# Optimization experiments

Hardware: AMD Instinct MI355X
Metric: run time of the kernel (lower is better)

The kernel has to match this reference:

```python
import jax, jax.numpy as jnp
import numpy as np

D = 512; N = 4096; NH = 16; DEPTH = 3; MLP = 4; GENES = 250; GH = 64; GW = 64


def setup_inputs() -> dict:
    key = jax.random.key(0)
    ks = jax.random.split(key, 10)
    gf = jax.random.normal(ks[0], (N, D), jnp.float32)
    # unique spot positions: permutation of the 64x64 grid cells
    perm = jax.random.permutation(ks[1], GH * GW)[:N]
    coords = jnp.stack([perm // GW, perm % GW], axis=1).astype(jnp.int32)
    s = 0.02
    rn = lambda k, sh: jax.random.normal(k, sh, jnp.float32) * s
    return dict(
        global_feats=gf, coords=coords, grid_h=GH, grid_w=GW,
        ln1_g=jnp.ones((DEPTH, D)), ln1_b=jnp.zeros((DEPTH, D)),
        wqkv=rn(ks[2], (DEPTH, 3 * D, D)), bqkv=jnp.zeros((DEPTH, 3 * D)),
        wo=rn(ks[3], (DEPTH, D, D)), bo=jnp.zeros((DEPTH, D)),
        ln2_g=jnp.ones((DEPTH, D)), ln2_b=jnp.zeros((DEPTH, D)),
        w1=rn(ks[4], (DEPTH, MLP * D, D)), b1=jnp.zeros((DEPTH, MLP * D)),
        w2=rn(ks[5], (DEPTH, D, MLP * D)), b2=jnp.zeros((DEPTH, D)),
        ck=rn(ks[6], (DEPTH, D, 1, 3, 3)), cb=jnp.zeros((DEPTH, D)),
        lnf_g=jnp.ones((D,)), lnf_b=jnp.zeros((D,)),
        wp=rn(ks[7], (GENES, D)), bp=jnp.zeros((GENES,)),
    )


def _ln(x, g, b, eps=1e-5):
    m = jnp.mean(x, axis=-1, keepdims=True)
    v = jnp.var(x, axis=-1, keepdims=True)
    return (x - m) * jax.lax.rsqrt(v + eps) * g + b


def reference(global_feats, coords, grid_h, grid_w, ln1_g, ln1_b, wqkv, bqkv,
              wo, bo, ln2_g, ln2_b, w1, b1, w2, b2, ck, cb, lnf_g, lnf_b, wp, bp):
    x = global_feats  # [N, D]
    n, d = x.shape
    nh = NH; dh = d // nh
    rows = coords[:, 0]; cols = coords[:, 1]
    for i in range(ln1_g.shape[0]):
        # --- self-attention (eval mode, dropout off) ---
        xn = _ln(x, ln1_g[i], ln1_b[i])
        qkv = xn @ wqkv[i].T + bqkv[i]                      # [N, 3D]
        q, k, v = jnp.split(qkv, 3, axis=-1)
        q = q.reshape(n, nh, dh).transpose(1, 0, 2)        # [H, N, dh]
        k = k.reshape(n, nh, dh).transpose(1, 0, 2)
        v = v.reshape(n, nh, dh).transpose(1, 0, 2)
        att = jax.nn.softmax(jnp.einsum('hqd,hkd->hqk', q, k) * (dh ** -0.5), axis=-1)
        ao = jnp.einsum('hqk,hkd->hqd', att, v).transpose(1, 0, 2).reshape(n, d)
        x = x + (ao @ wo[i].T + bo[i])
        # --- MLP ---
        h = jax.nn.gelu(_ln(x, ln2_g[i], ln2_b[i]) @ w1[i].T + b1[i], approximate=False)
        x = x + (h @ w2[i].T + b2[i])
        # --- APEG: scatter -> depthwise conv -> gather ---
        grid = jnp.zeros((d, grid_h, grid_w), x.dtype).at[:, rows, cols].set(x.T)
        co = jax.lax.conv_general_dilated(
            grid[None], ck[i], window_strides=(1, 1), padding=((1, 1), (1, 1)),
            dimension_numbers=('NCHW', 'OIHW', 'NCHW'), feature_group_count=d)[0]
        co = co + cb[i][:, None, None]
        x = x + co[:, rows, cols].T
    x = _ln(x, lnf_g, lnf_b)
    pred = x @ wp.T + bp
    return (x, pred)
```

## Files before the change

### kernel.cpp

```cpp
#include <hip/hip_runtime.h>
#include <math.h>

#define D 512
#define N_TOK 4096
#define NHEAD 16
#define DH 32
#define DEPTH 3
#define MLPD 2048
#define GENES 250
#define GH 64
#define GW 64

typedef __attribute__((ext_vector_type(8))) short short8;
typedef __attribute__((ext_vector_type(4))) float f32x4;
typedef unsigned short ushort_t;

#define AS1 __attribute__((address_space(1)))
#define AS3 __attribute__((address_space(3)))

#if defined(__has_builtin)
#if __has_builtin(__builtin_amdgcn_exp2f)
#define EXP2F(x) __builtin_amdgcn_exp2f(x)
#endif
#endif
#ifndef EXP2F
#define EXP2F(x) __expf(0.69314718056f * (x))
#endif

__device__ __forceinline__ unsigned short f2bf(float f) {
  unsigned int u = __float_as_uint(f);
  u += 0x7fffu + ((u >> 16) & 1u);
  return (unsigned short)(u >> 16);
}
__device__ __forceinline__ unsigned int bfpack(float a, float b) {
  return __builtin_amdgcn_perm(__float_as_uint(b), __float_as_uint(a), 0x07060302u);
}
__device__ __forceinline__ void gload_lds16(const ushort_t* g, ushort_t* l) {
  __builtin_amdgcn_global_load_lds(
      (const AS1 unsigned int*)g,
      (AS3 unsigned int*)(unsigned int)(unsigned long long)l, 16, 0, 0);
}
__device__ __forceinline__ int perm64(int m) {
  int mi = m >> 4, g = (m >> 2) & 3, r = m & 3;
  return ((mi & 1) << 5) | (g << 3) | ((mi >> 1) << 2) | r;
}

__global__ __launch_bounds__(256) void ln_kernel(const float* __restrict__ x,
    const float* __restrict__ g, const float* __restrict__ b,
    float* __restrict__ yf, ushort_t* __restrict__ ybf) {
  int row = blockIdx.x;
  int t = threadIdx.x;
  const float* xr = x + (size_t)row * D;
  float v0 = xr[t], v1 = xr[t + 256];
  float s = v0 + v1;
  float sq = v0 * v0 + v1 * v1;
#pragma unroll
  for (int off = 32; off > 0; off >>= 1) {
    s += __shfl_down(s, off, 64);
    sq += __shfl_down(sq, off, 64);
  }
  __shared__ float s1[4], s2[4];
  int wid = t >> 6, lane = t & 63;
  if (lane == 0) { s1[wid] = s; s2[wid] = sq; }
  __syncthreads();
  float tot = s1[0] + s1[1] + s1[2] + s1[3];
  float totq = s2[0] + s2[1] + s2[2] + s2[3];
  float mean = tot * (1.0f / D);
  float var = totq * (1.0f / D) - mean * mean;
  float rs = rsqrtf(var + 1e-5f);
  float r0 = (v0 - mean) * rs * g[t] + b[t];
  float r1 = (v1 - mean) * rs * g[t + 256] + b[t + 256];
  if (yf) { yf[(size_t)row * D + t] = r0; yf[(size_t)row * D + t + 256] = r1; }
  if (ybf) {
    ybf[(size_t)row * D + t] = f2bf(r0);
    ybf[(size_t)row * D + t + 256] = f2bf(r1);
  }
}

#define GBK 32

template <int TM, int TN>
__global__ __launch_bounds__(256) void gemm_bf(
    const ushort_t* __restrict__ A, const ushort_t* __restrict__ B,
    const float* __restrict__ bias, const float* __restrict__ res,
    float* __restrict__ C, ushort_t* __restrict__ Cbf,
    ushort_t* __restrict__ qO, ushort_t* __restrict__ kO, ushort_t* __restrict__ vO,
    int K, int ldc, int nstore, int mode) {
  constexpr int MI = TM / 32;
  constexpr int NI = TN / 32;
  __shared__ ushort_t As[TM * GBK];
  __shared__ ushort_t Bs[TN * GBK];
  int t = threadIdx.x;
  int w = t >> 6, lane = t & 63;
  int g = lane >> 4, c = lane & 15;
  int bm = blockIdx.y * TM, bn = blockIdx.x * TN;
  int wr = (w >> 1) * (TM / 2);
  int wc = (w & 1) * (TN / 2);

  const ushort_t* ga0 = A + (size_t)(bm + (t >> 2)) * K + (t & 3) * 8;
  const ushort_t* gb0 = B + (size_t)(bn + (t >> 2)) * K + (t & 3) * 8;
  const ushort_t* ga1 = A + (size_t)(bm + 64 + (t >> 2)) * K + (t & 3) * 8;
  const ushort_t* gb1 = B + (size_t)(bn + 64 + (t >> 2)) * K + (t & 3) * 8;
  ushort_t* la0 = As + t * 8;
  ushort_t* lb0 = Bs + t * 8;

  f32x4 acc[MI][NI] = {};

  for (int k0 = 0; k0 < K; k0 += GBK) {
    gload_lds16(ga0, la0);
    gload_lds16(gb0, lb0);
    if (TM == 128) gload_lds16(ga1, As + (t + 256) * 8);
    if (TN == 128) gload_lds16(gb1, Bs + (t + 256) * 8);
    ga0 += GBK; gb0 += GBK; ga1 += GBK; gb1 += GBK;
    __syncthreads();

    short8 af[MI], bfr[NI];
#pragma unroll
    for (int mi = 0; mi < MI; ++mi)
      af[mi] = *(const short8*)&As[(wr + mi * 16 + c) * GBK + g * 8];
#pragma unroll
    for (int ni = 0; ni < NI; ++ni)
      bfr[ni] = *(const short8*)&Bs[(wc + ni * 16 + c) * GBK + g * 8];
#pragma unroll
    for (int mi = 0; mi < MI; ++mi)
#pragma unroll
      for (int ni = 0; ni < NI; ++ni)
        acc[mi][ni] = __builtin_amdgcn_mfma_f32_16x16x32_bf16(
            af[mi], bfr[ni], acc[mi][ni], 0, 0, 0);
    __syncthreads();
  }

  const float qs_scale = 0.17677669529663688f * 1.4426950408889634f;
#pragma unroll
  for (int ni = 0; ni < NI; ++ni) {
    int col = bn + wc + ni * 16 + c;
    float bv = bias[col];
    bool cok = col < nstore;
#pragma unroll
    for (int mi = 0; mi < MI; ++mi) {
      int row0 = bm + wr + mi * 16 + g * 4;
#pragma unroll
      for (int reg = 0; reg < 4; ++reg) {
        int row = row0 + reg;
        float v = acc[mi][ni][reg] + bv;
        if (mode == 0) {
          size_t idx = (size_t)row * ldc + col;
          if (cok) {
            if (res) v += res[idx];
            C[idx] = v;
          }
        } else if (mode == 1) {
          v = 0.5f * v * (1.0f + erff(v * 0.70710678118654752f));
          Cbf[(size_t)row * ldc + col] = f2bf(v);
        } else {
          int which = col >> 9;
          int h = (col >> 5) & 15;
          int d = col & 31;
          size_t hb = (size_t)h * (N_TOK * DH);
          if (which == 0)
            qO[hb + (size_t)row * DH + d] = f2bf(v * qs_scale);
          else if (which == 1)
            kO[hb + (size_t)row * DH + d] = f2bf(v);
          else
            vO[hb + (size_t)d * N_TOK + ((row & ~63) | perm64(row & 63))] = f2bf(v);
        }
      }
    }
  }
}

#define KST 40
#define VTST 72

__global__ __launch_bounds__(256) void attn_mfma(
    const ushort_t* __restrict__ qb, const ushort_t* __restrict__ kb,
    const ushort_t* __restrict__ vtb, ushort_t* __restrict__ ao) {
  __shared__ ushort_t Ks[64 * KST];
  __shared__ ushort_t Vts[32 * VTST];
  int qt = blockIdx.x, head = blockIdx.y;
  int t = threadIdx.x;
  int w = t >> 6, lane = t & 63;
  int g = lane >> 4, c = lane & 15;
  const size_t hbase = (size_t)head * (N_TOK * DH);
  int q0 = qt * 128 + w * 32;

  short8 qf[2];
  qf[0] = *(const short8*)(qb + hbase + (size_t)(q0 + c) * DH + g * 8);
  qf[1] = *(const short8*)(qb + hbase + (size_t)(q0 + 16 + c) * DH + g * 8);

  short8 ones;
#pragma unroll
  for (int i = 0; i < 8; ++i) ones[i] = (short)0x3F80;

  f32x4 o[2][2] = {};
  f32x4 lf[2] = {};
  const f32x4 zf = {0.f, 0.f, 0.f, 0.f};

  const ushort_t* kg = kb + hbase + (size_t)(t >> 2) * DH + (t & 3) * 8;
  const ushort_t* vg = vtb + hbase + (size_t)(t >> 3) * N_TOK + (t & 7) * 8;
  ushort_t* kw = &Ks[(t >> 2) * KST + (t & 3) * 8];
  ushort_t* vw = &Vts[(t >> 3) * VTST + (t & 7) * 8];

  short8 kreg = *(const short8*)kg;
  short8 vreg = *(const short8*)vg;

  typedef union { short8 s8; unsigned int u32[4]; } pk_t;

  for (int tile = 0; tile < N_TOK / 64; ++tile) {
    __syncthreads();
    *(short8*)kw = kreg;
    *(short8*)vw = vreg;
    __syncthreads();
    if (tile + 1 < N_TOK / 64) {
      kreg = *(const short8*)(kg + (size_t)(tile + 1) * 64 * DH);
      vreg = *(const short8*)(vg + (tile + 1) * 64);
    }

    short8 kf[4];
#pragma unroll
    for (int mi = 0; mi < 4; ++mi)
      kf[mi] = *(const short8*)&Ks[(mi * 16 + c) * KST + g * 8];
    short8 vf[2][2];
#pragma unroll
    for (int half = 0; half < 2; ++half)
#pragma unroll
      for (int ch = 0; ch < 2; ++ch)
        vf[half][ch] = *(const short8*)&Vts[(half * 16 + c) * VTST + ch * 32 + g * 8];

    short8 pf[2][2];
#pragma unroll
    for (int qs = 0; qs < 2; ++qs) {
      f32x4 sp[4];
#pragma unroll
      for (int mi = 0; mi < 4; ++mi)
        sp[mi] = __builtin_amdgcn_mfma_f32_16x16x32_bf16(kf[mi], qf[qs], zf, 0, 0, 0);
      float pr[4][4];
#pragma unroll
      for (int mi = 0; mi < 4; ++mi)
#pragma unroll
        for (int r = 0; r < 4; ++r) pr[mi][r] = EXP2F(sp[mi][r]);
      pk_t p0, p1;
      p0.u32[0] = bfpack(pr[0][0], pr[0][1]);
      p0.u32[1] = bfpack(pr[0][2], pr[0][3]);
      p0.u32[2] = bfpack(pr[2][0], pr[2][1]);
      p0.u32[3] = bfpack(pr[2][2], pr[2][3]);
      p1.u32[0] = bfpack(pr[1][0], pr[1][1]);
      p1.u32[1] = bfpack(pr[1][2], pr[1][3]);
      p1.u32[2] = bfpack(pr[3][0], pr[3][1]);
      p1.u32[3] = bfpack(pr[3][2], pr[3][3]);
      pf[qs][0] = p0.s8;
      pf[qs][1] = p1.s8;
    }

#pragma unroll
    for (int qs = 0; qs < 2; ++qs) {
#pragma unroll
      for (int ch = 0; ch < 2; ++ch) {
        lf[qs] = __builtin_amdgcn_mfma_f32_16x16x32_bf16(ones, pf[qs][ch], lf[qs], 0, 0, 0);
#pragma unroll
        for (int half = 0; half < 2; ++half)
          o[qs][half] = __builtin_amdgcn_mfma_f32_16x16x32_bf16(
              vf[half][ch], pf[qs][ch], o[qs][half], 0, 0, 0);
      }
    }
  }

#pragma unroll
  for (int qs = 0; qs < 2; ++qs) {
    float inv = 1.0f / lf[qs][0];
    int q = q0 + qs * 16 + c;
    ushort_t* op = ao + (size_t)q * D + head * DH;
#pragma unroll
    for (int half = 0; half < 2; ++half)
#pragma unroll
      for (int reg = 0; reg < 4; ++reg)
        op[half * 16 + g * 4 + reg] = f2bf(o[qs][half][reg] * inv);
  }
}

__global__ void scatter_kernel(const int* __restrict__ coords,
                               int* __restrict__ pos2tok) {
  int n = blockIdx.x * 256 + threadIdx.x;
  if (n < N_TOK) pos2tok[coords[2 * n] * GW + coords[2 * n + 1]] = n;
}

__global__ __launch_bounds__(256) void conv_ln_kernel(
    const float* __restrict__ xin, float* __restrict__ xout,
    const float* __restrict__ ck, const float* __restrict__ cb,
    const int* __restrict__ pos2tok, const int* __restrict__ coords,
    const float* __restrict__ g, const float* __restrict__ b,
    float* __restrict__ yf, ushort_t* __restrict__ ybf) {
  int n = blockIdx.x, t = threadIdx.x;
  __shared__ int nb[9];
  if (t < 9) {
    int r = coords[2 * n], c = coords[2 * n + 1];
    int dy = t / 3 - 1, dx = t % 3 - 1;
    int rr = r + dy, cc = c + dx;
    nb[t] = (rr >= 0 && rr < GH && cc >= 0 && cc < GW) ? pos2tok[rr * GW + cc] : -1;
  }
  __syncthreads();
  float v[2];
#pragma unroll
  for (int j = 0; j < 2; ++j) {
    int ch = t + j * 256;
    float s = cb[ch];
#pragma unroll
    for (int tap = 0; tap < 9; ++tap) {
      int tok = nb[tap];
      if (tok >= 0) s = fmaf(ck[ch * 9 + tap], xin[(size_t)tok * D + ch], s);
    }
    v[j] = xin[(size_t)n * D + ch] + s;
    xout[(size_t)n * D + ch] = v[j];
  }
  float s = v[0] + v[1];
  float sq = v[0] * v[0] + v[1] * v[1];
#pragma unroll
  for (int off = 32; off > 0; off >>= 1) {
    s += __shfl_down(s, off, 64);
    sq += __shfl_down(sq, off, 64);
  }
  __shared__ float s1[4], s2[4];
  int wid = t >> 6, lane = t & 63;
  if (lane == 0) { s1[wid] = s; s2[wid] = sq; }
  __syncthreads();
  float tot = s1[0] + s1[1] + s1[2] + s1[3];
  float totq = s2[0] + s2[1] + s2[2] + s2[3];
  float mean = tot * (1.0f / D);
  float var = totq * (1.0f / D) - mean * mean;
  float rs = rsqrtf(var + 1e-5f);
  float r0 = (v[0] - mean) * rs * g[t] + b[t];
  float r1 = (v[1] - mean) * rs * g[t + 256] + b[t + 256];
  if (yf) { yf[(size_t)n * D + t] = r0; yf[(size_t)n * D + t + 256] = r1; }
  ybf[(size_t)n * D + t] = f2bf(r0);
  ybf[(size_t)n * D + t + 256] = f2bf(r1);
}

__global__ __launch_bounds__(256) void castw(const float* __restrict__ src,
    ushort_t* __restrict__ dst, int n_src, int n_dst) {
  int i = (blockIdx.x * 256 + threadIdx.x) * 4;
  if (i >= n_dst) return;
  unsigned long long pk = 0;
#pragma unroll
  for (int j = 0; j < 4; ++j) {
    float v = (i + j < n_src) ? src[i + j] : 0.f;
    pk |= ((unsigned long long)f2bf(v)) << (16 * j);
  }
  *(unsigned long long*)(dst + i) = pk;
}

__global__ void pad_bias(const float* __restrict__ src, float* __restrict__ dst) {
  int i = threadIdx.x;
  dst[i] = (i < GENES) ? src[i] : 0.f;
}

extern "C" void kernel_launch(void* const* d_in, const int* in_sizes, int n_in,
                              void* d_out, int out_size, void* d_ws, size_t ws_size,
                              hipStream_t stream) {
  const float* gf     = (const float*)d_in[0];
  const int*   coords = (const int*)d_in[1];
  const float* ln1_g  = (const float*)d_in[4];
  const float* ln1_b  = (const float*)d_in[5];
  const float* wqkv   = (const float*)d_in[6];
  const float* bqkv   = (const float*)d_in[7];
  const float* wo     = (const float*)d_in[8];
  const float* bo     = (const float*)d_in[9];
  const float* ln2_g  = (const float*)d_in[10];
  const float* ln2_b  = (const float*)d_in[11];
  const float* w1     = (const float*)d_in[12];
  const float* b1     = (const float*)d_in[13];
  const float* w2     = (const float*)d_in[14];
  const float* b2     = (const float*)d_in[15];
  const float* ck     = (const float*)d_in[16];
  const float* cb     = (const float*)d_in[17];
  const float* lnf_g  = (const float*)d_in[18];
  const float* lnf_b  = (const float*)d_in[19];
  const float* wp     = (const float*)d_in[20];
  const float* bp     = (const float*)d_in[21];
  float* out = (float*)d_out;

  const size_t ND = (size_t)N_TOK * D;
  float* xb0 = (float*)d_ws;
  float* xb1 = xb0 + ND;
  ushort_t* xn_bf  = (ushort_t*)(xb1 + ND);
  ushort_t* ao_bf  = xn_bf + ND;
  ushort_t* out_bf = ao_bf + ND;
  ushort_t* shared = out_bf + ND;
  ushort_t* qb   = shared;
  ushort_t* kbuf = qb + ND;
  ushort_t* vtb  = kbuf + ND;
  ushort_t* h_bf = shared;
  ushort_t* wqkv_bf = shared + (size_t)N_TOK * MLPD;
  ushort_t* wo_bf = wqkv_bf + DEPTH * 3 * D * D;
  ushort_t* w1_bf = wo_bf + DEPTH * D * D;
  ushort_t* w2_bf = w1_bf + DEPTH * MLPD * D;
  ushort_t* wp_bf = w2_bf + DEPTH * D * MLPD;
  float* bp_pad = (float*)(wp_bf + 256 * D);
  int* pos2tok = (int*)(bp_pad + 256);

  hipMemcpyAsync(xb0, gf, ND * sizeof(float), hipMemcpyDeviceToDevice, stream);
  hipMemsetAsync(pos2tok, 0xFF, GH * GW * sizeof(int), stream);
  scatter_kernel<<<(N_TOK + 255) / 256, 256, 0, stream>>>(coords, pos2tok);

  int nw;
  nw = DEPTH * 3 * D * D;  castw<<<(nw / 4 + 255) / 256, 256, 0, stream>>>(wqkv, wqkv_bf, nw, nw);
  nw = DEPTH * D * D;      castw<<<(nw / 4 + 255) / 256, 256, 0, stream>>>(wo, wo_bf, nw, nw);
  nw = DEPTH * MLPD * D;   castw<<<(nw / 4 + 255) / 256, 256, 0, stream>>>(w1, w1_bf, nw, nw);
  nw = DEPTH * D * MLPD;   castw<<<(nw / 4 + 255) / 256, 256, 0, stream>>>(w2, w2_bf, nw, nw);
  castw<<<(256 * D / 4 + 255) / 256, 256, 0, stream>>>(wp, wp_bf, GENES * D, 256 * D);
  pad_bias<<<1, 256, 0, stream>>>(bp, bp_pad);

  ln_kernel<<<N_TOK, 256, 0, stream>>>(xb0, ln1_g, ln1_b, nullptr, xn_bf);

  float* x  = xb0;
  float* xo = xb1;
  for (int i = 0; i < DEPTH; ++i) {
    gemm_bf<128, 128><<<dim3(12, 32), 256, 0, stream>>>(
        xn_bf, wqkv_bf + (size_t)i * 3 * D * D, bqkv + (size_t)i * 3 * D,
        nullptr, nullptr, nullptr, qb, kbuf, vtb, D, 0, 3 * D, 2);
    attn_mfma<<<dim3(N_TOK / 128, NHEAD), 256, 0, stream>>>(qb, kbuf, vtb, ao_bf);
    gemm_bf<64, 64><<<dim3(8, 64), 256, 0, stream>>>(
        ao_bf, wo_bf + (size_t)i * D * D, bo + (size_t)i * D,
        x, x, nullptr, nullptr, nullptr, nullptr, D, D, D, 0);
    ln_kernel<<<N_TOK, 256, 0, stream>>>(x, ln2_g + i * D, ln2_b + i * D, nullptr, xn_bf);
    gemm_bf<128, 128><<<dim3(16, 32), 256, 0, stream>>>(
        xn_bf, w1_bf + (size_t)i * MLPD * D, b1 + (size_t)i * MLPD,
        nullptr, nullptr, h_bf, nullptr, nullptr, nullptr, D, MLPD, MLPD, 1);
    gemm_bf<64, 64><<<dim3(8, 64), 256, 0, stream>>>(
        h_bf, w2_bf + (size_t)i * D * MLPD, b2 + (size_t)i * D,
        x, x, nullptr, nullptr, nullptr, nullptr, MLPD, D, D, 0);
    if (i < DEPTH - 1) {
      conv_ln_kernel<<<N_TOK, 256, 0, stream>>>(
          x, xo, ck + (size_t)i * D * 9, cb + (size_t)i * D, pos2tok, coords,
          ln1_g + (i + 1) * D, ln1_b + (i + 1) * D, nullptr, xn_bf);
    } else {
      conv_ln_kernel<<<N_TOK, 256, 0, stream>>>(
          x, xo, ck + (size_t)i * D * 9, cb + (size_t)i * D, pos2tok, coords,
          lnf_g, lnf_b, out, out_bf);
    }
    float* tmp = x; x = xo; xo = tmp;
  }
  gemm_bf<64, 64><<<dim3(4, 64), 256, 0, stream>>>(
      out_bf, wp_bf, bp_pad, nullptr, out + ND, nullptr, nullptr, nullptr, nullptr,
      D, GENES, GENES, 0);
}
```

Measured before the change: 714.4 us.

## Double-buffer GEMM LDS tiles and vectorize V-transpose stores in QKV epilogue

Turns the bf16 GEMM main loop into a double-buffered pipeline. The global-to-LDS loads for the next K tile are issued before the MFMAs on the current one, leaving one barrier per iteration instead of two. The 64x64 GEMMs stage two K halves (64 wide) per buffer to cut loop and sync overhead. The QKV epilogue is split into its own path that packs four bf16 V values into a single 8-byte store using the inlined permutation, in exchange for doubled LDS use and more code complexity.

After: 624.2 us. -12.6%, faster.

```diff
diff --git a/kernel.cpp b/kernel.cpp
--- a/kernel.cpp
+++ b/kernel.cpp
@@ -77,9 +77,7 @@
   }
 }
 
-#define GBK 32
-
-template <int TM, int TN>
+template <int TM, int TN, int NKH>
 __global__ __launch_bounds__(256) void gemm_bf(
     const ushort_t* __restrict__ A, const ushort_t* __restrict__ B,
     const float* __restrict__ bias, const float* __restrict__ res,
@@ -88,8 +86,8 @@
     int K, int ldc, int nstore, int mode) {
   constexpr int MI = TM / 32;
   constexpr int NI = TN / 32;
-  __shared__ ushort_t As[TM * GBK];
-  __shared__ ushort_t Bs[TN * GBK];
+  __shared__ ushort_t As[2][NKH][TM * 32];
+  __shared__ ushort_t Bs[2][NKH][TN * 32];
   int t = threadIdx.x;
   int w = t >> 6, lane = t & 63;
   int g = lane >> 4, c = lane & 15;
@@ -97,40 +95,88 @@
   int wr = (w >> 1) * (TM / 2);
   int wc = (w & 1) * (TN / 2);
 
-  const ushort_t* ga0 = A + (size_t)(bm + (t >> 2)) * K + (t & 3) * 8;
-  const ushort_t* gb0 = B + (size_t)(bn + (t >> 2)) * K + (t & 3) * 8;
-  const ushort_t* ga1 = A + (size_t)(bm + 64 + (t >> 2)) * K + (t & 3) * 8;
-  const ushort_t* gb1 = B + (size_t)(bn + 64 + (t >> 2)) * K + (t & 3) * 8;
-  ushort_t* la0 = As + t * 8;
-  ushort_t* lb0 = Bs + t * 8;
+  const ushort_t* gA = A + (size_t)(bm + (t >> 2)) * K + (t & 3) * 8;
+  const ushort_t* gB = B + (size_t)(bn + (t >> 2)) * K + (t & 3) * 8;
+
+  auto stage = [&](int p, int koff) {
+#pragma unroll
+    for (int h = 0; h < NKH; ++h) {
+      gload_lds16(gA + koff + h * 32, &As[p][h][t * 8]);
+      if (TM == 128)
+        gload_lds16(gA + koff + h * 32 + (size_t)64 * K, &As[p][h][(t + 256) * 8]);
+      gload_lds16(gB + koff + h * 32, &Bs[p][h][t * 8]);
+      if (TN == 128)
+        gload_lds16(gB + koff + h * 32 + (size_t)64 * K, &Bs[p][h][(t + 256) * 8]);
+    }
+  };
 
   f32x4 acc[MI][NI] = {};
 
-  for (int k0 = 0; k0 < K; k0 += GBK) {
-    gload_lds16(ga0, la0);
-    gload_lds16(gb0, lb0);
-    if (TM == 128) gload_lds16(ga1, As + (t + 256) * 8);
-    if (TN == 128) gload_lds16(gb1, Bs + (t + 256) * 8);
-    ga0 += GBK; gb0 += GBK; ga1 += GBK; gb1 += GBK;
+  const int niter = K / (32 * NKH);
+  stage(0, 0);
+  __syncthreads();
+  for (int it = 0; it < niter; ++it) {
+    int p = it & 1;
+    if (it + 1 < niter) stage(p ^ 1, (it + 1) * 32 * NKH);
+#pragma unroll
+    for (int kh = 0; kh < NKH; ++kh) {
+      short8 af[MI], bfr[NI];
+#pragma unroll
+      for (int mi = 0; mi < MI; ++mi)
+        af[mi] = *(const short8*)&As[p][kh][(wr + mi * 16 + c) * 32 + g * 8];
+#pragma unroll
+      for (int ni = 0; ni < NI; ++ni)
+        bfr[ni] = *(const short8*)&Bs[p][kh][(wc + ni * 16 + c) * 32 + g * 8];
+#pragma unroll
+      for (int mi = 0; mi < MI; ++mi)
+#pragma unroll
+        for (int ni = 0; ni < NI; ++ni)
+          acc[mi][ni] = __builtin_amdgcn_mfma_f32_16x16x32_bf16(
+              af[mi], bfr[ni], acc[mi][ni], 0, 0, 0);
+    }
     __syncthreads();
-
-    short8 af[MI], bfr[NI];
-#pragma unroll
-    for (int mi = 0; mi < MI; ++mi)
-      af[mi] = *(const short8*)&As[(wr + mi * 16 + c) * GBK + g * 8];
-#pragma unroll
-    for (int ni = 0; ni < NI; ++ni)
-      bfr[ni] = *(const short8*)&Bs[(wc + ni * 16 + c) * GBK + g * 8];
-#pragma unroll
-    for (int mi = 0; mi < MI; ++mi)
-#pragma unroll
-      for (int ni = 0; ni < NI; ++ni)
-        acc[mi][ni] = __builtin_amdgcn_mfma_f32_16x16x32_bf16(
-            af[mi], bfr[ni], acc[mi][ni], 0, 0, 0);
-    __syncthreads();
   }
 
   const float qs_scale = 0.17677669529663688f * 1.4426950408889634f;
+  if (mode == 2) {
+#pragma unroll
+    for (int ni = 0; ni < NI; ++ni) {
+      int col = bn + wc + ni * 16 + c;
+      float bv = bias[col];
+      int which = col >> 9;
+      int h = (col >> 5) & 15;
+      int d = col & 31;
+      size_t hb = (size_t)h * (N_TOK * DH);
+#pragma unroll
+      for (int mi = 0; mi < MI; ++mi) {
+        int row0 = bm + wr + mi * 16 + g * 4;
+        float v0 = acc[mi][ni][0] + bv;
+        float v1 = acc[mi][ni][1] + bv;
+        float v2 = acc[mi][ni][2] + bv;
+        float v3 = acc[mi][ni][3] + bv;
+        if (which == 0) {
+          qO[hb + (size_t)(row0 + 0) * DH + d] = f2bf(v0 * qs_scale);
+          qO[hb + (size_t)(row0 + 1) * DH + d] = f2bf(v1 * qs_scale);
+          qO[hb + (size_t)(row0 + 2) * DH + d] = f2bf(v2 * qs_scale);
+          qO[hb + (size_t)(row0 + 3) * DH + d] = f2bf(v3 * qs_scale);
+        } else if (which == 1) {
+          kO[hb + (size_t)(row0 + 0) * DH + d] = f2bf(v0);
+          kO[hb + (size_t)(row0 + 1) * DH + d] = f2bf(v1);
+          kO[hb + (size_t)(row0 + 2) * DH + d] = f2bf(v2);
+          kO[hb + (size_t)(row0 + 3) * DH + d] = f2bf(v3);
+        } else {
+          int m = row0 & 63;
+          int mi_l = m >> 4, g_l = (m >> 2) & 3;
+          int nb = ((mi_l & 1) << 5) | (g_l << 3) | ((mi_l >> 1) << 2);
+          uint2 pk;
+          pk.x = (unsigned)f2bf(v0) | ((unsigned)f2bf(v1) << 16);
+          pk.y = (unsigned)f2bf(v2) | ((unsigned)f2bf(v3) << 16);
+          *(uint2*)(vO + hb + (size_t)d * N_TOK + (row0 & ~63) + nb) = pk;
+        }
+      }
+    }
+    return;
+  }
 #pragma unroll
   for (int ni = 0; ni < NI; ++ni) {
     int col = bn + wc + ni * 16 + c;
@@ -149,20 +195,9 @@
             if (res) v += res[idx];
             C[idx] = v;
           }
-        } else if (mode == 1) {
+        } else {
           v = 0.5f * v * (1.0f + erff(v * 0.70710678118654752f));
           Cbf[(size_t)row * ldc + col] = f2bf(v);
-        } else {
-          int which = col >> 9;
-          int h = (col >> 5) & 15;
-          int d = col & 31;
-          size_t hb = (size_t)h * (N_TOK * DH);
-          if (which == 0)
-            qO[hb + (size_t)row * DH + d] = f2bf(v * qs_scale);
-          else if (which == 1)
-            kO[hb + (size_t)row * DH + d] = f2bf(v);
-          else
-            vO[hb + (size_t)d * N_TOK + ((row & ~63) | perm64(row & 63))] = f2bf(v);
         }
       }
     }
@@ -414,18 +449,18 @@
   float* x  = xb0;
   float* xo = xb1;
   for (int i = 0; i < DEPTH; ++i) {
-    gemm_bf<128, 128><<<dim3(12, 32), 256, 0, stream>>>(
+    gemm_bf<128, 128, 1><<<dim3(12, 32), 256, 0, stream>>>(
         xn_bf, wqkv_bf + (size_t)i * 3 * D * D, bqkv + (size_t)i * 3 * D,
         nullptr, nullptr, nullptr, qb, kbuf, vtb, D, 0, 3 * D, 2);
     attn_mfma<<<dim3(N_TOK / 128, NHEAD), 256, 0, stream>>>(qb, kbuf, vtb, ao_bf);
-    gemm_bf<64, 64><<<dim3(8, 64), 256, 0, stream>>>(
+    gemm_bf<64, 64, 2><<<dim3(8, 64), 256, 0, stream>>>(
         ao_bf, wo_bf + (size_t)i * D * D, bo + (size_t)i * D,
         x, x, nullptr, nullptr, nullptr, nullptr, D, D, D, 0);
     ln_kernel<<<N_TOK, 256, 0, stream>>>(x, ln2_g + i * D, ln2_b + i * D, nullptr, xn_bf);
-    gemm_bf<128, 128><<<dim3(16, 32), 256, 0, stream>>>(
+    gemm_bf<128, 128, 1><<<dim3(16, 32), 256, 0, stream>>>(
         xn_bf, w1_bf + (size_t)i * MLPD * D, b1 + (size_t)i * MLPD,
         nullptr, nullptr, h_bf, nullptr, nullptr, nullptr, D, MLPD, MLPD, 1);
-    gemm_bf<64, 64><<<dim3(8, 64), 256, 0, stream>>>(
+    gemm_bf<64, 64, 2><<<dim3(8, 64), 256, 0, stream>>>(
         h_bf, w2_bf + (size_t)i * D * MLPD, b2 + (size_t)i * D,
         x, x, nullptr, nullptr, nullptr, nullptr, MLPD, D, D, 0);
     if (i < DEPTH - 1) {
@@ -439,7 +474,7 @@
     }
     float* tmp = x; x = xo; xo = tmp;
   }
-  gemm_bf<64, 64><<<dim3(4, 64), 256, 0, stream>>>(
+  gemm_bf<64, 64, 2><<<dim3(4, 64), 256, 0, stream>>>(
       out_bf, wp_bf, bp_pad, nullptr, out + ND, nullptr, nullptr, nullptr, nullptr,
       D, GENES, GENES, 0);
 }
```
